# Performance work log

Hardware: AMD Instinct MI355X
Metric: run time of the kernel (lower is better)

## Reference

```python
import jax, jax.numpy as jnp
import numpy as np

N_G, E_G = 50000, 800000
N_S, E_S = 10000, 160000
NF = 64
B = 8

def _w(key, shape):
    fan_in = shape[-1]
    return jax.random.normal(key, shape, dtype=jnp.float32) / np.sqrt(fan_in)

def setup_inputs() -> dict:
    key = jax.random.key(0)
    ks = jax.random.split(key, 40)
    inp = {
        "graph_x": jax.random.normal(ks[0], (N_G, NF), dtype=jnp.float32),
        "subgraph_x": jax.random.normal(ks[1], (N_S, NF), dtype=jnp.float32),
        "point": jax.random.normal(ks[2], (B, NF), dtype=jnp.float32),
        "graph_edge_index": jax.random.randint(ks[3], (2, E_G), 0, N_G),
        "graph_batch": jnp.sort(jax.random.randint(ks[4], (N_G,), 0, B)),
        "subgraph_edge_index": jax.random.randint(ks[5], (2, E_S), 0, N_S),
        "subgraph_batch": jnp.sort(jax.random.randint(ks[6], (N_S,), 0, B)),
    }
    # GraphConv params per branch: channel sizes 64->128->256->192
    dims = [(2 * NF, NF), (4 * NF, 2 * NF), (3 * NF, 4 * NF)]
    i = 7
    for pre in ("g", "s"):
        for li, (o, c) in enumerate(dims, start=1):
            inp[f"{pre}W{li}r"] = _w(ks[i], (o, c)); i += 1  # lin_rel (aggregated)
            inp[f"{pre}W{li}n"] = _w(ks[i], (o, c)); i += 1  # lin_root (self)
            inp[f"{pre}B{li}"] = jnp.zeros((o,), dtype=jnp.float32)
    inp["l1W"] = _w(ks[i], (600, 3 * NF + 3 * NF + NF)); i += 1
    inp["l1b"] = jnp.zeros((600,), dtype=jnp.float32)
    inp["l2W"] = _w(ks[i], (256, 600)); i += 1
    inp["l2b"] = jnp.zeros((256,), dtype=jnp.float32)
    inp["l3W"] = _w(ks[i], (NF, 256)); i += 1
    inp["l3b"] = jnp.zeros((NF,), dtype=jnp.float32)
    return inp

def _graph_conv(x, src, dst, Wr, Wn, b, n_nodes):
    # PyG GraphConv: out_i = Wr @ sum_{j->i} x_j + Wn @ x_i + b
    agg = jax.ops.segment_sum(x[src], dst, num_segments=n_nodes)
    return agg @ Wr.T + x @ Wn.T + b

def _scatter_mean(x, seg, num_segments):
    s = jax.ops.segment_sum(x, seg, num_segments=num_segments)
    cnt = jax.ops.segment_sum(jnp.ones((x.shape[0],), x.dtype), seg, num_segments=num_segments)
    return s / jnp.maximum(cnt, 1.0)[:, None]

def _branch(x, edge_index, batch, params, n_nodes):
    src, dst = edge_index[0], edge_index[1]
    for (Wr, Wn, b) in params:
        x = jax.nn.elu(_graph_conv(x, src, dst, Wr, Wn, b, n_nodes))
    return _scatter_mean(x, batch, B)

def reference(graph_x, subgraph_x, point,
              gW1r, gW1n, gB1, gW2r, gW2n, gB2, gW3r, gW3n, gB3,
              sW1r, sW1n, sB1, sW2r, sW2n, sB2, sW3r, sW3n, sB3,
              l1W, l1b, l2W, l2b, l3W, l3b,
              graph_edge_index, graph_batch, subgraph_edge_index, subgraph_batch):
    x1 = _branch(graph_x, graph_edge_index, graph_batch,
                 [(gW1r, gW1n, gB1), (gW2r, gW2n, gB2), (gW3r, gW3n, gB3)], N_G)
    x2 = _branch(subgraph_x, subgraph_edge_index, subgraph_batch,
                 [(sW1r, sW1n, sB1), (sW2r, sW2n, sB2), (sW3r, sW3n, sB3)], N_S)
    x = jnp.concatenate([x1, x2, point], axis=-1)  # [B, 448]
    x = jax.nn.relu(x @ l1W.T + l1b)
    x = jax.nn.relu(x @ l2W.T + l2b)
    return x @ l3W.T + l3b  # [B, 64]
```

## Files before the change

kernel.cpp:

```cpp
#include <hip/hip_runtime.h>
#include <cmath>

typedef __attribute__((ext_vector_type(8))) short short8;
typedef __attribute__((ext_vector_type(4))) short shortx4;
typedef __attribute__((ext_vector_type(4))) float floatx4;
typedef __attribute__((ext_vector_type(2))) float floatx2;
typedef __attribute__((ext_vector_type(4))) int intx4;

#define N_G 50000
#define E_G 800000
#define N_S 10000
#define E_S 160000
#define NT (N_G + N_S)
#define ET (E_G + E_S)
#define BATCH 8
#define STRIDE 64
#define FPASS 8

__device__ __forceinline__ float b2f(short s) {
    unsigned u = ((unsigned)(unsigned short)s) << 16;
    return __builtin_bit_cast(float, u);
}
__device__ __forceinline__ short f2b(float f) {
    unsigned u = __builtin_bit_cast(unsigned, f);
    u += 0x7FFF + ((u >> 16) & 1);
    return (short)(u >> 16);
}

struct RepArgs { const float* Wr[6]; const float* Wn[6]; short* dst[6]; int cin[6]; int nk[6]; int groups[6]; };
__global__ void init_kernel(const float* __restrict__ gx, const float* __restrict__ sx,
                            short* __restrict__ X0, unsigned char* __restrict__ X0_8,
                            int* __restrict__ dcount, float* __restrict__ pooled,
                            const int* __restrict__ g_batch, const int* __restrict__ s_batch,
                            int* __restrict__ starts, RepArgs ra, int total_groups) {
    int t = blockIdx.x * blockDim.x + threadIdx.x;
    if (t < NT * 16) {
        size_t e = (size_t)t * 4;
        const float* src = (e < (size_t)N_G * 64) ? (gx + e) : (sx + (e - (size_t)N_G * 64));
        floatx4 v = *(const floatx4*)src;
        shortx4 o;
        o[0] = f2b(v[0]); o[1] = f2b(v[1]); o[2] = f2b(v[2]); o[3] = f2b(v[3]);
        *(shortx4*)(X0 + e) = o;
        int w8 = 0;
        w8 = __builtin_amdgcn_cvt_pk_fp8_f32(v[0], v[1], w8, false);
        w8 = __builtin_amdgcn_cvt_pk_fp8_f32(v[2], v[3], w8, true);
        *(unsigned int*)(X0_8 + e) = (unsigned int)w8;
    }
    if (t < NT) dcount[t] = 0;
    if (t < 16 * 192) pooled[t] = 0.f;
    if (t <= 16) {
        int b = t;
        if (b == 16) { starts[16] = NT; }
        else {
            int key, n, base;
            const int* arr;
            if (b < 8) { arr = g_batch; n = N_G; key = b; base = 0; }
            else       { arr = s_batch; n = N_S; key = b - 8; base = N_G; }
            int lo = 0, hi = n;
            while (lo < hi) { int mid = (lo + hi) >> 1; if (arr[mid] < key) lo = mid + 1; else hi = mid; }
            starts[b] = base + lo;
        }
    }
    if (t < total_groups) {
        int seg = 0, off = t;
        while (seg < 5 && off >= ra.groups[seg]) { off -= ra.groups[seg]; ++seg; }
        int CIN = ra.cin[seg], NK = ra.nk[seg];
        int lane = off & 63;
        int rest = off >> 6;
        int tt = rest % NK;
        int ot = rest / NK;
        int o = ot * 16 + (lane & 15);
        int kk = tt * 32 + (lane >> 4) * 8;
        const float* src = (kk < CIN) ? (ra.Wr[seg] + (size_t)o * CIN + kk)
                                      : (ra.Wn[seg] + (size_t)o * CIN + (kk - CIN));
        floatx4 u0 = *(const floatx4*)src;
        floatx4 u1 = *(const floatx4*)(src + 4);
        short8 d;
        d[0]=f2b(u0[0]); d[1]=f2b(u0[1]); d[2]=f2b(u0[2]); d[3]=f2b(u0[3]);
        d[4]=f2b(u1[0]); d[5]=f2b(u1[1]); d[6]=f2b(u1[2]); d[7]=f2b(u1[3]);
        *(short8*)(ra.dst[seg] + (size_t)off * 8) = d;
    }
}

__global__ void fill_kernel(const int* __restrict__ g_ei, const int* __restrict__ s_ei,
                            int* __restrict__ dcount, int* __restrict__ csr) {
    int pass = blockIdx.x & (FPASS - 1);
    int lb   = blockIdx.x >> 3;
    int t = lb * blockDim.x + threadIdx.x;
    if (t >= ET) return;
    int dst;
    if (t < E_G) dst = g_ei[E_G + t];
    else         dst = s_ei[E_S + (t - E_G)] + N_G;
    int lo = pass * (NT / FPASS);
    int hi = lo + (NT / FPASS);
    if (dst < lo || dst >= hi) return;
    int src;
    if (t < E_G) src = g_ei[t];
    else         src = s_ei[t - E_G] + N_G;
    int slot = atomicAdd(&dcount[dst], 1);
    if (slot < STRIDE) csr[(size_t)dst * STRIDE + slot] = src;
}

template<int C>
__global__ void agg8_kernel(const unsigned char* __restrict__ x8, const int* __restrict__ dcount,
                            const int* __restrict__ csr, short* __restrict__ out) {
    constexpr int C16 = C / 16;
    int t = blockIdx.x * blockDim.x + threadIdx.x;
    if (t >= NT * C16) return;
    int node = t / C16;
    int ch   = t % C16;
    int e0 = node * STRIDE;
    int e1 = e0 + min(dcount[node], STRIDE);
    float acc[16];
    #pragma unroll
    for (int j = 0; j < 16; ++j) acc[j] = 0.f;
    for (int e = e0; e < e1; ++e) {
        int s = csr[e];
        intx4 w = *(const intx4*)(x8 + (size_t)s * C + ch * 16);
        #pragma unroll
        for (int q = 0; q < 4; ++q) {
            floatx2 f0 = __builtin_amdgcn_cvt_pk_f32_fp8(w[q], false);
            floatx2 f1 = __builtin_amdgcn_cvt_pk_f32_fp8(w[q], true);
            acc[q * 4 + 0] += f0[0];
            acc[q * 4 + 1] += f0[1];
            acc[q * 4 + 2] += f1[0];
            acc[q * 4 + 3] += f1[1];
        }
    }
    short8 o0, o1;
    #pragma unroll
    for (int j = 0; j < 8; ++j) { o0[j] = f2b(acc[j]); o1[j] = f2b(acc[8 + j]); }
    short8* q = (short8*)(out + (size_t)node * C + ch * 16);
    q[0] = o0; q[1] = o1;
}

template<int CIN, int COUT, bool POOL>
__global__ __launch_bounds__(256) void gemm_elu_kernel(
        const short* __restrict__ A1, const short* __restrict__ A2,
        const short* __restrict__ gWF, const short* __restrict__ sWF,
        const float* __restrict__ gB, const float* __restrict__ sB,
        short* __restrict__ out, unsigned char* __restrict__ out8,
        float* __restrict__ pooled, const int* __restrict__ starts) {
    constexpr int NK  = CIN / 16;
    constexpr int NOT = COUT / 16;
    int wave = (blockIdx.x * blockDim.x + threadIdx.x) >> 6;
    int lane = threadIdx.x & 63;
    int r0 = wave * 16;
    if (r0 >= NT) return;
    bool sub = (r0 >= N_G);
    const short* WF = sub ? sWF : gWF;
    const float* bias = sub ? sB : gB;
    int id = lane & 15, quad = lane >> 4;
    int arow = r0 + id;
    short8 a[NK];
    #pragma unroll
    for (int t = 0; t < NK; ++t) {
        int kk = t * 32 + quad * 8;
        const short* p = (kk < CIN) ? (A1 + (size_t)arow * CIN + kk)
                                    : (A2 + (size_t)arow * CIN + (kk - CIN));
        a[t] = *(const short8*)p;
    }
    int seg0 = 0, seg1 = 0;
    bool uniform = true;
    if (POOL) {
        while (seg0 < 15 && starts[seg0 + 1] <= r0) ++seg0;
        seg1 = seg0;
        while (seg1 < 15 && starts[seg1 + 1] <= r0 + 15) ++seg1;
        uniform = (seg0 == seg1);
    }
    for (int ot = 0; ot < NOT; ++ot) {
        floatx4 acc = {0.f, 0.f, 0.f, 0.f};
        const short* wp = WF + (((size_t)ot * NK) * 64 + lane) * 8;
        #pragma unroll
        for (int t = 0; t < NK; ++t) {
            short8 b = *(const short8*)(wp + (size_t)t * 64 * 8);
            acc = __builtin_amdgcn_mfma_f32_16x16x32_bf16(a[t], b, acc, 0, 0, 0);
        }
        int o = ot * 16 + id;
        float bv = bias[o];
        float vr[4];
        #pragma unroll
        for (int r = 0; r < 4; ++r) {
            float v = acc[r] + bv;
            vr[r] = (v > 0.f) ? v : (expf(v) - 1.f);
        }
        if (!POOL) {
            #pragma unroll
            for (int r = 0; r < 4; ++r) {
                int nrow = r0 + quad * 4 + r;
                out[(size_t)nrow * COUT + o] = f2b(vr[r]);
                if (out8) {
                    int w8 = __builtin_amdgcn_cvt_pk_fp8_f32(vr[r], vr[r], 0, false);
                    out8[(size_t)nrow * COUT + o] = (unsigned char)(w8 & 0xFF);
                }
            }
        } else if (uniform) {
            float vsum = vr[0] + vr[1] + vr[2] + vr[3];
            vsum += __shfl_down(vsum, 32, 64);
            vsum += __shfl_down(vsum, 16, 64);
            if (lane < 16) atomicAdd(&pooled[seg0 * 192 + o], vsum);
        } else {
            #pragma unroll
            for (int r = 0; r < 4; ++r) {
                int nrow = r0 + quad * 4 + r;
                int sg = seg0;
                while (sg < seg1 && starts[sg + 1] <= nrow) ++sg;
                atomicAdd(&pooled[sg * 192 + o], vr[r]);
            }
        }
    }
}

__global__ void build_in_kernel(const float* __restrict__ pooled, const int* __restrict__ starts,
                                const float* __restrict__ point, float* __restrict__ mlp_in) {
    int t = blockIdx.x * blockDim.x + threadIdx.x;
    if (t >= BATCH * 448) return;
    int b = t / 448, j = t % 448;
    float v;
    if (j < 192) {
        int c = starts[b + 1] - starts[b];
        v = pooled[b * 192 + j] / (float)max(c, 1);
    } else if (j < 384) {
        int c = starts[9 + b] - starts[8 + b];
        v = pooled[(8 + b) * 192 + (j - 192)] / (float)max(c, 1);
    } else {
        v = point[b * 64 + (j - 384)];
    }
    mlp_in[t] = v;
}

__global__ __launch_bounds__(256) void dense_wave_kernel(
        const float* __restrict__ in, const float* __restrict__ W,
        const float* __restrict__ bias, float* __restrict__ out,
        int I, int O, int relu) {
    int wave = (blockIdx.x * blockDim.x + threadIdx.x) >> 6;
    int lane = threadIdx.x & 63;
    if (wave >= BATCH * O) return;
    int b = wave / O, o = wave % O;
    const float* x = in + (size_t)b * I;
    const float* w = W + (size_t)o * I;
    float acc = 0.f;
    for (int i = lane; i < I; i += 64) acc += x[i] * w[i];
    #pragma unroll
    for (int off = 32; off > 0; off >>= 1) acc += __shfl_down(acc, off, 64);
    if (lane == 0) {
        acc += bias[o];
        if (relu) acc = fmaxf(acc, 0.f);
        out[wave] = acc;
    }
}

extern "C" void kernel_launch(void* const* d_in, const int* in_sizes, int n_in,
                              void* d_out, int out_size, void* d_ws, size_t ws_size,
                              hipStream_t stream) {
    const float* graph_x = (const float*)d_in[0];
    const float* sub_x   = (const float*)d_in[1];
    const float* point   = (const float*)d_in[2];
    const int*   g_ei    = (const int*)d_in[3];
    const int*   g_batch = (const int*)d_in[4];
    const int*   s_ei    = (const int*)d_in[5];
    const int*   s_batch = (const int*)d_in[6];
    const float* gB1=(const float*)d_in[9],  *gB2=(const float*)d_in[12], *gB3=(const float*)d_in[15];
    const float* sB1=(const float*)d_in[18], *sB2=(const float*)d_in[21], *sB3=(const float*)d_in[24];
    const float* l1W=(const float*)d_in[25], *l1b=(const float*)d_in[26];
    const float* l2W=(const float*)d_in[27], *l2b=(const float*)d_in[28];
    const float* l3W=(const float*)d_in[29], *l3b=(const float*)d_in[30];

    char* ws = (char*)d_ws;
    size_t off = 0;
    auto alloc = [&](size_t bytes) -> char* {
        char* p = ws + off;
        off = (off + bytes + 255) & ~(size_t)255;
        return p;
    };
    int* dcount = (int*)alloc((size_t)NT * 4);
    int* csr = (int*)alloc((size_t)NT * STRIDE * 4);

    const int fsz[3] = {128 * 2 * 64, 256 * 2 * 128, 192 * 2 * 256};
    short* wfrag = (short*)alloc((size_t)(fsz[0] + fsz[1] + fsz[2]) * 2 * 2);
    short* gWF[3], *sWF[3];
    { size_t o2 = 0;
      for (int l = 0; l < 3; ++l) { gWF[l] = wfrag + o2; o2 += fsz[l]; }
      for (int l = 0; l < 3; ++l) { sWF[l] = wfrag + o2; o2 += fsz[l]; } }

    short* X0  = (short*)alloc((size_t)NT * 64 * 2);
    unsigned char* X0_8 = (unsigned char*)alloc((size_t)NT * 64);
    short* agg = (short*)alloc((size_t)NT * 256 * 2);
    short* h1  = (short*)alloc((size_t)NT * 128 * 2);
    short* h2  = (short*)alloc((size_t)NT * 256 * 2);
    unsigned char* h1_8 = (unsigned char*)alloc((size_t)NT * 128);
    unsigned char* h2_8 = (unsigned char*)alloc((size_t)NT * 256);

    float* pooled = (float*)alloc(16 * 192 * 4);
    int* starts = (int*)alloc(17 * 4);
    float* mlp_in = (float*)alloc(BATCH * 448 * 4);
    float* mlp_h1 = (float*)alloc(BATCH * 600 * 4);
    float* mlp_h2 = (float*)alloc(BATCH * 256 * 4);

    RepArgs ra;
    const int cin_l[3] = {64, 128, 256};
    const int nk_l[3]  = {4, 8, 16};
    const int not_l[3] = {8, 16, 12};
    const int wr_idx[6] = {7, 10, 13, 16, 19, 22};
    int total_groups = 0;
    for (int s = 0; s < 6; ++s) {
        int l = s % 3;
        ra.Wr[s] = (const float*)d_in[wr_idx[s]];
        ra.Wn[s] = (const float*)d_in[wr_idx[s] + 1];
        ra.dst[s] = (s < 3) ? gWF[l] : sWF[l];
        ra.cin[s] = cin_l[l];
        ra.nk[s] = nk_l[l];
        ra.groups[s] = not_l[l] * nk_l[l] * 64;
        total_groups += ra.groups[s];
    }

    init_kernel<<<(NT * 16 + 255) / 256, 256, 0, stream>>>(graph_x, sub_x, X0, X0_8, dcount,
                                                           pooled, g_batch, s_batch, starts,
                                                           ra, total_groups);

    fill_kernel<<<((ET + 255) / 256) * FPASS, 256, 0, stream>>>(g_ei, s_ei, dcount, csr);

    constexpr int NW = NT / 16;
    const int gemm_blocks = (NW + 3) / 4;

    agg8_kernel<64><<<(NT * 4 + 255) / 256, 256, 0, stream>>>(X0_8, dcount, csr, agg);
    gemm_elu_kernel<64, 128, false><<<gemm_blocks, 256, 0, stream>>>(agg, X0, gWF[0], sWF[0], gB1, sB1, h1, h1_8, nullptr, nullptr);
    agg8_kernel<128><<<(NT * 8 + 255) / 256, 256, 0, stream>>>(h1_8, dcount, csr, agg);
    gemm_elu_kernel<128, 256, false><<<gemm_blocks, 256, 0, stream>>>(agg, h1, gWF[1], sWF[1], gB2, sB2, h2, h2_8, nullptr, nullptr);
    agg8_kernel<256><<<(NT * 16 + 255) / 256, 256, 0, stream>>>(h2_8, dcount, csr, agg);
    gemm_elu_kernel<256, 192, true><<<gemm_blocks, 256, 0, stream>>>(agg, h2, gWF[2], sWF[2], gB3, sB3, nullptr, nullptr, pooled, starts);

    build_in_kernel<<<(BATCH * 448 + 255) / 256, 256, 0, stream>>>(pooled, starts, point, mlp_in);
    dense_wave_kernel<<<(BATCH * 600 + 3) / 4, 256, 0, stream>>>(mlp_in, l1W, l1b, mlp_h1, 448, 600, 1);
    dense_wave_kernel<<<(BATCH * 256 + 3) / 4, 256, 0, stream>>>(mlp_h1, l2W, l2b, mlp_h2, 600, 256, 1);
    dense_wave_kernel<<<(BATCH * 64 + 3) / 4, 256, 0, stream>>>(mlp_h2, l3W, l3b, (float*)d_out, 256, 64, 0);
}
```

Baseline: 391.4 us.

## Stage GraphConv weight tiles in LDS and split output channels across grid

Replaces the per-wave GEMM, which streamed every weight fragment from global memory for each 16-row tile, with a kernel that copies a slice of output-channel weights into shared memory once per block. Each wave now handles two row tiles. The grid is split over output-channel groups (y) and over the graph/subgraph branch (z). This is meant to cut repeated global weight traffic and raise reuse of each loaded weight fragment. In exchange, the A rows are reloaded once per channel group, and the launch bound of one block per SM plus larger register arrays may lower occupancy.

```diff
diff --git a/kernel.cpp b/kernel.cpp
--- a/kernel.cpp
+++ b/kernel.cpp
@@ -134,78 +134,99 @@
     q[0] = o0; q[1] = o1;
 }
 
-template<int CIN, int COUT, bool POOL>
-__global__ __launch_bounds__(256) void gemm_elu_kernel(
+template<int CIN, int COUT, int OTN, int RPW, bool POOL>
+__global__ __launch_bounds__(256, 1) void gemm_lds_kernel(
         const short* __restrict__ A1, const short* __restrict__ A2,
         const short* __restrict__ gWF, const short* __restrict__ sWF,
         const float* __restrict__ gB, const float* __restrict__ sB,
         short* __restrict__ out, unsigned char* __restrict__ out8,
         float* __restrict__ pooled, const int* __restrict__ starts) {
-    constexpr int NK  = CIN / 16;
-    constexpr int NOT = COUT / 16;
-    int wave = (blockIdx.x * blockDim.x + threadIdx.x) >> 6;
-    int lane = threadIdx.x & 63;
-    int r0 = wave * 16;
-    if (r0 >= NT) return;
-    bool sub = (r0 >= N_G);
-    const short* WF = sub ? sWF : gWF;
-    const float* bias = sub ? sB : gB;
+    constexpr int NK = CIN / 16;
+    __shared__ short lds[OTN * NK * 512];
+    int z = blockIdx.z;
+    const short* WF = z ? sWF : gWF;
+    const float* bias = z ? sB : gB;
+    int rowBase  = z ? N_G : 0;
+    int rowTiles = z ? (N_S / 16) : (N_G / 16);
+    int rtBase = blockIdx.x * (4 * RPW);
+    if (rtBase >= rowTiles) return;
+    const short* wsrc = WF + ((size_t)(blockIdx.y * OTN) * NK) * 512;
+    for (int i = threadIdx.x; i < OTN * NK * 64; i += 256)
+        *(short8*)(lds + (size_t)i * 8) = *(const short8*)(wsrc + (size_t)i * 8);
+    __syncthreads();
+    int wv = threadIdx.x >> 6, lane = threadIdx.x & 63;
     int id = lane & 15, quad = lane >> 4;
-    int arow = r0 + id;
-    short8 a[NK];
+    int rt[RPW]; bool act[RPW];
+    short8 a[RPW][NK];
     #pragma unroll
-    for (int t = 0; t < NK; ++t) {
-        int kk = t * 32 + quad * 8;
-        const short* p = (kk < CIN) ? (A1 + (size_t)arow * CIN + kk)
-                                    : (A2 + (size_t)arow * CIN + (kk - CIN));
-        a[t] = *(const short8*)p;
-    }
-    int seg0 = 0, seg1 = 0;
-    bool uniform = true;
+    for (int r = 0; r < RPW; ++r) {
+        rt[r] = rtBase + wv * RPW + r;
+        act[r] = rt[r] < rowTiles;
+        int arow = rowBase + (act[r] ? rt[r] : 0) * 16 + id;
+        #pragma unroll
+        for (int t = 0; t < NK; ++t) {
+            int kk = t * 32 + quad * 8;
+            const short* p = (kk < CIN) ? (A1 + (size_t)arow * CIN + kk)
+                                        : (A2 + (size_t)arow * CIN + (kk - CIN));
+            a[r][t] = *(const short8*)p;
+        }
+    }
+    int seg0[RPW], seg1[RPW];
     if (POOL) {
-        while (seg0 < 15 && starts[seg0 + 1] <= r0) ++seg0;
-        seg1 = seg0;
-        while (seg1 < 15 && starts[seg1 + 1] <= r0 + 15) ++seg1;
-        uniform = (seg0 == seg1);
-    }
-    for (int ot = 0; ot < NOT; ++ot) {
-        floatx4 acc = {0.f, 0.f, 0.f, 0.f};
-        const short* wp = WF + (((size_t)ot * NK) * 64 + lane) * 8;
-        #pragma unroll
-        for (int t = 0; t < NK; ++t) {
-            short8 b = *(const short8*)(wp + (size_t)t * 64 * 8);
-            acc = __builtin_amdgcn_mfma_f32_16x16x32_bf16(a[t], b, acc, 0, 0, 0);
-        }
-        int o = ot * 16 + id;
+        #pragma unroll
+        for (int r = 0; r < RPW; ++r) {
+            int r0 = rowBase + (act[r] ? rt[r] : 0) * 16;
+            int s0 = 0;
+            while (s0 < 15 && starts[s0 + 1] <= r0) ++s0;
+            int s1 = s0;
+            while (s1 < 15 && starts[s1 + 1] <= r0 + 15) ++s1;
+            seg0[r] = s0; seg1[r] = s1;
+        }
+    }
+    for (int oi = 0; oi < OTN; ++oi) {
+        short8 b[NK];
+        #pragma unroll
+        for (int t = 0; t < NK; ++t)
+            b[t] = *(const short8*)(lds + (((size_t)(oi * NK + t)) * 64 + lane) * 8);
+        int o = (blockIdx.y * OTN + oi) * 16 + id;
         float bv = bias[o];
-        float vr[4];
-        #pragma unroll
-        for (int r = 0; r < 4; ++r) {
-            float v = acc[r] + bv;
-            vr[r] = (v > 0.f) ? v : (expf(v) - 1.f);
-        }
-        if (!POOL) {
+        #pragma unroll
+        for (int r = 0; r < RPW; ++r) {
+            if (!act[r]) continue;
+            floatx4 acc = {0.f, 0.f, 0.f, 0.f};
             #pragma unroll
-            for (int r = 0; r < 4; ++r) {
-                int nrow = r0 + quad * 4 + r;
-                out[(size_t)nrow * COUT + o] = f2b(vr[r]);
-                if (out8) {
-                    int w8 = __builtin_amdgcn_cvt_pk_fp8_f32(vr[r], vr[r], 0, false);
-                    out8[(size_t)nrow * COUT + o] = (unsigned char)(w8 & 0xFF);
+            for (int t = 0; t < NK; ++t)
+                acc = __builtin_amdgcn_mfma_f32_16x16x32_bf16(a[r][t], b[t], acc, 0, 0, 0);
+            float vr[4];
+            #pragma unroll
+            for (int q = 0; q < 4; ++q) {
+                float v = acc[q] + bv;
+                vr[q] = (v > 0.f) ? v : (expf(v) - 1.f);
+            }
+            int r0 = rowBase + rt[r] * 16;
+            if (!POOL) {
+                #pragma unroll
+                for (int q = 0; q < 4; ++q) {
+                    int nrow = r0 + quad * 4 + q;
+                    out[(size_t)nrow * COUT + o] = f2b(vr[q]);
+                    if (out8) {
+                        int w8 = __builtin_amdgcn_cvt_pk_fp8_f32(vr[q], vr[q], 0, false);
+                        out8[(size_t)nrow * COUT + o] = (unsigned char)(w8 & 0xFF);
+                    }
                 }
-            }
-        } else if (uniform) {
-            float vsum = vr[0] + vr[1] + vr[2] + vr[3];
-            vsum += __shfl_down(vsum, 32, 64);
-            vsum += __shfl_down(vsum, 16, 64);
-            if (lane < 16) atomicAdd(&pooled[seg0 * 192 + o], vsum);
-        } else {
-            #pragma unroll
-            for (int r = 0; r < 4; ++r) {
-                int nrow = r0 + quad * 4 + r;
-                int sg = seg0;
-                while (sg < seg1 && starts[sg + 1] <= nrow) ++sg;
-                atomicAdd(&pooled[sg * 192 + o], vr[r]);
+            } else if (seg0[r] == seg1[r]) {
+                float vsum = vr[0] + vr[1] + vr[2] + vr[3];
+                vsum += __shfl_down(vsum, 32, 64);
+                vsum += __shfl_down(vsum, 16, 64);
+                if (lane < 16) atomicAdd(&pooled[seg0[r] * 192 + o], vsum);
+            } else {
+                #pragma unroll
+                for (int q = 0; q < 4; ++q) {
+                    int nrow = r0 + quad * 4 + q;
+                    int sg = seg0[r];
+                    while (sg < seg1[r] && starts[sg + 1] <= nrow) ++sg;
+                    atomicAdd(&pooled[sg * 192 + o], vr[q]);
+                }
             }
         }
     }
@@ -320,15 +341,17 @@
 
     fill_kernel<<<((ET + 255) / 256) * FPASS, 256, 0, stream>>>(g_ei, s_ei, dcount, csr);
 
-    constexpr int NW = NT / 16;
-    const int gemm_blocks = (NW + 3) / 4;
+    const int gx = (3125 + 7) / 8;
 
     agg8_kernel<64><<<(NT * 4 + 255) / 256, 256, 0, stream>>>(X0_8, dcount, csr, agg);
-    gemm_elu_kernel<64, 128, false><<<gemm_blocks, 256, 0, stream>>>(agg, X0, gWF[0], sWF[0], gB1, sB1, h1, h1_8, nullptr, nullptr);
+    gemm_lds_kernel<64, 128, 8, 2, false><<<dim3(gx, 1, 2), 256, 0, stream>>>(
+        agg, X0, gWF[0], sWF[0], gB1, sB1, h1, h1_8, nullptr, nullptr);
     agg8_kernel<128><<<(NT * 8 + 255) / 256, 256, 0, stream>>>(h1_8, dcount, csr, agg);
-    gemm_elu_kernel<128, 256, false><<<gemm_blocks, 256, 0, stream>>>(agg, h1, gWF[1], sWF[1], gB2, sB2, h2, h2_8, nullptr, nullptr);
+    gemm_lds_kernel<128, 256, 8, 2, false><<<dim3(gx, 2, 2), 256, 0, stream>>>(
+        agg, h1, gWF[1], sWF[1], gB2, sB2, h2, h2_8, nullptr, nullptr);
     agg8_kernel<256><<<(NT * 16 + 255) / 256, 256, 0, stream>>>(h2_8, dcount, csr, agg);
-    gemm_elu_kernel<256, 192, true><<<gemm_blocks, 256, 0, stream>>>(agg, h2, gWF[2], sWF[2], gB3, sB3, nullptr, nullptr, pooled, starts);
+    gemm_lds_kernel<256, 192, 4, 2, true><<<dim3(gx, 3, 2), 256, 0, stream>>>(
+        agg, h2, gWF[2], sWF[2], gB3, sB3, nullptr, nullptr, pooled, starts);
 
     build_in_kernel<<<(BATCH * 448 + 255) / 256, 256, 0, stream>>>(pooled, starts, point, mlp_in);
     dense_wave_kernel<<<(BATCH * 600 + 3) / 4, 256, 0, stream>>>(mlp_in, l1W, l1b, mlp_h1, 448, 600, 1);
```

New measurement: 410.4 us. 4.9% more time.

## Fuse neighbor aggregation into GEMM+ELU kernel via shared-memory staging

Applied to the files above, without the earlier changes.

Merges each layer's separate fp8 gather-aggregation kernel and bf16 MFMA GEMM kernel into one kernel. Per 64-row block, threads aggregate neighbor features into LDS, optionally stage the self features in LDS too, sync, then run the MFMA/ELU epilogue from LDS. This removes the global agg buffer round trip and three kernel launches. In exchange, each block's aggregation and GEMM phases are serialized, and the larger LDS footprint may lower occupancy.

```diff
diff --git a/kernel.cpp b/kernel.cpp
--- a/kernel.cpp
+++ b/kernel.cpp
@@ -101,72 +101,84 @@
     if (slot < STRIDE) csr[(size_t)dst * STRIDE + slot] = src;
 }
 
-template<int C>
-__global__ void agg8_kernel(const unsigned char* __restrict__ x8, const int* __restrict__ dcount,
-                            const int* __restrict__ csr, short* __restrict__ out) {
-    constexpr int C16 = C / 16;
-    int t = blockIdx.x * blockDim.x + threadIdx.x;
-    if (t >= NT * C16) return;
-    int node = t / C16;
-    int ch   = t % C16;
-    int e0 = node * STRIDE;
-    int e1 = e0 + min(dcount[node], STRIDE);
-    float acc[16];
-    #pragma unroll
-    for (int j = 0; j < 16; ++j) acc[j] = 0.f;
-    for (int e = e0; e < e1; ++e) {
-        int s = csr[e];
-        intx4 w = *(const intx4*)(x8 + (size_t)s * C + ch * 16);
-        #pragma unroll
-        for (int q = 0; q < 4; ++q) {
-            floatx2 f0 = __builtin_amdgcn_cvt_pk_f32_fp8(w[q], false);
-            floatx2 f1 = __builtin_amdgcn_cvt_pk_f32_fp8(w[q], true);
-            acc[q * 4 + 0] += f0[0];
-            acc[q * 4 + 1] += f0[1];
-            acc[q * 4 + 2] += f1[0];
-            acc[q * 4 + 3] += f1[1];
-        }
-    }
-    short8 o0, o1;
-    #pragma unroll
-    for (int j = 0; j < 8; ++j) { o0[j] = f2b(acc[j]); o1[j] = f2b(acc[8 + j]); }
-    short8* q = (short8*)(out + (size_t)node * C + ch * 16);
-    q[0] = o0; q[1] = o1;
-}
-
 template<int CIN, int COUT, bool POOL>
-__global__ __launch_bounds__(256) void gemm_elu_kernel(
-        const short* __restrict__ A1, const short* __restrict__ A2,
+__global__ __launch_bounds__(256) void fused_layer_kernel(
+        const unsigned char* __restrict__ x8, const short* __restrict__ hprev,
+        const int* __restrict__ dcount, const int* __restrict__ csr,
         const short* __restrict__ gWF, const short* __restrict__ sWF,
         const float* __restrict__ gB, const float* __restrict__ sB,
         short* __restrict__ out, unsigned char* __restrict__ out8,
         float* __restrict__ pooled, const int* __restrict__ starts) {
-    constexpr int NK  = CIN / 16;
-    constexpr int NOT = COUT / 16;
-    int wave = (blockIdx.x * blockDim.x + threadIdx.x) >> 6;
-    int lane = threadIdx.x & 63;
-    int r0 = wave * 16;
+    constexpr int NK   = CIN / 16;
+    constexpr int NOT  = COUT / 16;
+    constexpr bool STA2 = (CIN <= 128);
+    constexpr int WP   = STA2 ? (2 * CIN + 8) : (CIN + 8);
+    __shared__ short lds[64 * WP];
+    int rowBase = blockIdx.x * 64;
+    int tid = threadIdx.x;
+    constexpr int CH = CIN / 16;
+    for (int item = tid; item < 64 * CH; item += 256) {
+        int row = item / CH, ch = item % CH;
+        int grow = rowBase + row;
+        if (grow >= NT) continue;
+        int e0 = grow * STRIDE;
+        int e1 = e0 + min(dcount[grow], STRIDE);
+        float acc[16];
+        #pragma unroll
+        for (int j = 0; j < 16; ++j) acc[j] = 0.f;
+        for (int e = e0; e < e1; ++e) {
+            int s = csr[e];
+            intx4 w = *(const intx4*)(x8 + (size_t)s * CIN + ch * 16);
+            #pragma unroll
+            for (int q = 0; q < 4; ++q) {
+                floatx2 f0 = __builtin_amdgcn_cvt_pk_f32_fp8(w[q], false);
+                floatx2 f1 = __builtin_amdgcn_cvt_pk_f32_fp8(w[q], true);
+                acc[q * 4 + 0] += f0[0];
+                acc[q * 4 + 1] += f0[1];
+                acc[q * 4 + 2] += f1[0];
+                acc[q * 4 + 3] += f1[1];
+            }
+        }
+        short8 o0, o1;
+        #pragma unroll
+        for (int j = 0; j < 8; ++j) { o0[j] = f2b(acc[j]); o1[j] = f2b(acc[8 + j]); }
+        short* p = lds + row * WP + ch * 16;
+        *(short8*)p = o0;
+        *(short8*)(p + 8) = o1;
+    }
+    if (STA2) {
+        constexpr int CH2 = CIN / 8;
+        for (int item = tid; item < 64 * CH2; item += 256) {
+            int row = item / CH2, ch = item % CH2;
+            int grow = rowBase + row;
+            if (grow >= NT) continue;
+            *(short8*)(lds + row * WP + CIN + ch * 8) =
+                *(const short8*)(hprev + (size_t)grow * CIN + ch * 8);
+        }
+    }
+    __syncthreads();
+    int wv = tid >> 6, lane = tid & 63;
+    int r0 = rowBase + wv * 16;
     if (r0 >= NT) return;
     bool sub = (r0 >= N_G);
     const short* WF = sub ? sWF : gWF;
     const float* bias = sub ? sB : gB;
     int id = lane & 15, quad = lane >> 4;
-    int arow = r0 + id;
+    int lrow = wv * 16 + id;
     short8 a[NK];
     #pragma unroll
     for (int t = 0; t < NK; ++t) {
         int kk = t * 32 + quad * 8;
-        const short* p = (kk < CIN) ? (A1 + (size_t)arow * CIN + kk)
-                                    : (A2 + (size_t)arow * CIN + (kk - CIN));
-        a[t] = *(const short8*)p;
+        if (STA2 || kk < CIN)
+            a[t] = *(const short8*)(lds + lrow * WP + kk);
+        else
+            a[t] = *(const short8*)(hprev + (size_t)(r0 + id) * CIN + (kk - CIN));
     }
     int seg0 = 0, seg1 = 0;
-    bool uniform = true;
     if (POOL) {
         while (seg0 < 15 && starts[seg0 + 1] <= r0) ++seg0;
         seg1 = seg0;
         while (seg1 < 15 && starts[seg1 + 1] <= r0 + 15) ++seg1;
-        uniform = (seg0 == seg1);
     }
     for (int ot = 0; ot < NOT; ++ot) {
         floatx4 acc = {0.f, 0.f, 0.f, 0.f};
@@ -189,12 +201,10 @@
             for (int r = 0; r < 4; ++r) {
                 int nrow = r0 + quad * 4 + r;
                 out[(size_t)nrow * COUT + o] = f2b(vr[r]);
-                if (out8) {
-                    int w8 = __builtin_amdgcn_cvt_pk_fp8_f32(vr[r], vr[r], 0, false);
-                    out8[(size_t)nrow * COUT + o] = (unsigned char)(w8 & 0xFF);
-                }
+                int w8 = __builtin_amdgcn_cvt_pk_fp8_f32(vr[r], vr[r], 0, false);
+                out8[(size_t)nrow * COUT + o] = (unsigned char)(w8 & 0xFF);
             }
-        } else if (uniform) {
+        } else if (seg0 == seg1) {
             float vsum = vr[0] + vr[1] + vr[2] + vr[3];
             vsum += __shfl_down(vsum, 32, 64);
             vsum += __shfl_down(vsum, 16, 64);
@@ -285,7 +295,6 @@
 
     short* X0  = (short*)alloc((size_t)NT * 64 * 2);
     unsigned char* X0_8 = (unsigned char*)alloc((size_t)NT * 64);
-    short* agg = (short*)alloc((size_t)NT * 256 * 2);
     short* h1  = (short*)alloc((size_t)NT * 128 * 2);
     short* h2  = (short*)alloc((size_t)NT * 256 * 2);
     unsigned char* h1_8 = (unsigned char*)alloc((size_t)NT * 128);
@@ -320,15 +329,14 @@
 
     fill_kernel<<<((ET + 255) / 256) * FPASS, 256, 0, stream>>>(g_ei, s_ei, dcount, csr);
 
-    constexpr int NW = NT / 16;
-    const int gemm_blocks = (NW + 3) / 4;
-
-    agg8_kernel<64><<<(NT * 4 + 255) / 256, 256, 0, stream>>>(X0_8, dcount, csr, agg);
-    gemm_elu_kernel<64, 128, false><<<gemm_blocks, 256, 0, stream>>>(agg, X0, gWF[0], sWF[0], gB1, sB1, h1, h1_8, nullptr, nullptr);
-    agg8_kernel<128><<<(NT * 8 + 255) / 256, 256, 0, stream>>>(h1_8, dcount, csr, agg);
-    gemm_elu_kernel<128, 256, false><<<gemm_blocks, 256, 0, stream>>>(agg, h1, gWF[1], sWF[1], gB2, sB2, h2, h2_8, nullptr, nullptr);
-    agg8_kernel<256><<<(NT * 16 + 255) / 256, 256, 0, stream>>>(h2_8, dcount, csr, agg);
-    gemm_elu_kernel<256, 192, true><<<gemm_blocks, 256, 0, stream>>>(agg, h2, gWF[2], sWF[2], gB3, sB3, nullptr, nullptr, pooled, starts);
+    const int gx = (NT + 63) / 64;
+
+    fused_layer_kernel<64, 128, false><<<gx, 256, 0, stream>>>(
+        X0_8, X0, dcount, csr, gWF[0], sWF[0], gB1, sB1, h1, h1_8, nullptr, nullptr);
+    fused_layer_kernel<128, 256, false><<<gx, 256, 0, stream>>>(
+        h1_8, h1, dcount, csr, gWF[1], sWF[1], gB2, sB2, h2, h2_8, nullptr, nullptr);
+    fused_layer_kernel<256, 192, true><<<gx, 256, 0, stream>>>(
+        h2_8, h2, dcount, csr, gWF[2], sWF[2], gB3, sB3, nullptr, nullptr, pooled, starts);
 
     build_in_kernel<<<(BATCH * 448 + 255) / 256, 256, 0, stream>>>(pooled, starts, point, mlp_in);
     dense_wave_kernel<<<(BATCH * 600 + 3) / 4, 256, 0, stream>>>(mlp_in, l1W, l1b, mlp_h1, 448, 600, 1);
```

After: 395.3 us. About the same (+1.0%).

## Drop bf16 activation copies, read root features from fp8, fuse MLP input build

Applied to the files above, without the earlier changes.

The GEMM kernels now read the self/root operand from the fp8 activation buffers and convert it to bf16 in registers. The separate bf16 copies of X0, h1 and h2 are no longer written or read, which cuts global memory traffic. The build_in kernel is folded into the first MLP layer, saving one launch. The trade-off is lower precision on the root term, which was bf16 before and is now fp8, plus extra conversion instructions in the GEMM.

```diff
diff --git a/kernel.cpp b/kernel.cpp
--- a/kernel.cpp
+++ b/kernel.cpp
@@ -6,6 +6,7 @@
 typedef __attribute__((ext_vector_type(4))) float floatx4;
 typedef __attribute__((ext_vector_type(2))) float floatx2;
 typedef __attribute__((ext_vector_type(4))) int intx4;
+typedef __attribute__((ext_vector_type(2))) int intx2;
 
 #define N_G 50000
 #define E_G 800000
@@ -26,10 +27,20 @@
     u += 0x7FFF + ((u >> 16) & 1);
     return (short)(u >> 16);
 }
+__device__ __forceinline__ short8 fp8x8_to_bf16(intx2 w) {
+    floatx2 f0 = __builtin_amdgcn_cvt_pk_f32_fp8(w[0], false);
+    floatx2 f1 = __builtin_amdgcn_cvt_pk_f32_fp8(w[0], true);
+    floatx2 f2 = __builtin_amdgcn_cvt_pk_f32_fp8(w[1], false);
+    floatx2 f3 = __builtin_amdgcn_cvt_pk_f32_fp8(w[1], true);
+    short8 r;
+    r[0]=f2b(f0[0]); r[1]=f2b(f0[1]); r[2]=f2b(f1[0]); r[3]=f2b(f1[1]);
+    r[4]=f2b(f2[0]); r[5]=f2b(f2[1]); r[6]=f2b(f3[0]); r[7]=f2b(f3[1]);
+    return r;
+}
 
 struct RepArgs { const float* Wr[6]; const float* Wn[6]; short* dst[6]; int cin[6]; int nk[6]; int groups[6]; };
 __global__ void init_kernel(const float* __restrict__ gx, const float* __restrict__ sx,
-                            short* __restrict__ X0, unsigned char* __restrict__ X0_8,
+                            unsigned char* __restrict__ X0_8,
                             int* __restrict__ dcount, float* __restrict__ pooled,
                             const int* __restrict__ g_batch, const int* __restrict__ s_batch,
                             int* __restrict__ starts, RepArgs ra, int total_groups) {
@@ -38,9 +49,6 @@
         size_t e = (size_t)t * 4;
         const float* src = (e < (size_t)N_G * 64) ? (gx + e) : (sx + (e - (size_t)N_G * 64));
         floatx4 v = *(const floatx4*)src;
-        shortx4 o;
-        o[0] = f2b(v[0]); o[1] = f2b(v[1]); o[2] = f2b(v[2]); o[3] = f2b(v[3]);
-        *(shortx4*)(X0 + e) = o;
         int w8 = 0;
         w8 = __builtin_amdgcn_cvt_pk_fp8_f32(v[0], v[1], w8, false);
         w8 = __builtin_amdgcn_cvt_pk_fp8_f32(v[2], v[3], w8, true);
@@ -136,10 +144,10 @@
 
 template<int CIN, int COUT, bool POOL>
 __global__ __launch_bounds__(256) void gemm_elu_kernel(
-        const short* __restrict__ A1, const short* __restrict__ A2,
+        const short* __restrict__ A1, const unsigned char* __restrict__ A2_8,
         const short* __restrict__ gWF, const short* __restrict__ sWF,
         const float* __restrict__ gB, const float* __restrict__ sB,
-        short* __restrict__ out, unsigned char* __restrict__ out8,
+        unsigned char* __restrict__ out8,
         float* __restrict__ pooled, const int* __restrict__ starts) {
     constexpr int NK  = CIN / 16;
     constexpr int NOT = COUT / 16;
@@ -156,17 +164,18 @@
     #pragma unroll
     for (int t = 0; t < NK; ++t) {
         int kk = t * 32 + quad * 8;
-        const short* p = (kk < CIN) ? (A1 + (size_t)arow * CIN + kk)
-                                    : (A2 + (size_t)arow * CIN + (kk - CIN));
-        a[t] = *(const short8*)p;
+        if (kk < CIN) {
+            a[t] = *(const short8*)(A1 + (size_t)arow * CIN + kk);
+        } else {
+            intx2 w = *(const intx2*)(A2_8 + (size_t)arow * CIN + (kk - CIN));
+            a[t] = fp8x8_to_bf16(w);
+        }
     }
     int seg0 = 0, seg1 = 0;
-    bool uniform = true;
     if (POOL) {
         while (seg0 < 15 && starts[seg0 + 1] <= r0) ++seg0;
         seg1 = seg0;
         while (seg1 < 15 && starts[seg1 + 1] <= r0 + 15) ++seg1;
-        uniform = (seg0 == seg1);
     }
     for (int ot = 0; ot < NOT; ++ot) {
         floatx4 acc = {0.f, 0.f, 0.f, 0.f};
@@ -188,13 +197,10 @@
             #pragma unroll
             for (int r = 0; r < 4; ++r) {
                 int nrow = r0 + quad * 4 + r;
-                out[(size_t)nrow * COUT + o] = f2b(vr[r]);
-                if (out8) {
-                    int w8 = __builtin_amdgcn_cvt_pk_fp8_f32(vr[r], vr[r], 0, false);
-                    out8[(size_t)nrow * COUT + o] = (unsigned char)(w8 & 0xFF);
-                }
+                int w8 = __builtin_amdgcn_cvt_pk_fp8_f32(vr[r], vr[r], 0, false);
+                out8[(size_t)nrow * COUT + o] = (unsigned char)(w8 & 0xFF);
             }
-        } else if (uniform) {
+        } else if (seg0 == seg1) {
             float vsum = vr[0] + vr[1] + vr[2] + vr[3];
             vsum += __shfl_down(vsum, 32, 64);
             vsum += __shfl_down(vsum, 16, 64);
@@ -211,22 +217,28 @@
     }
 }
 
-__global__ void build_in_kernel(const float* __restrict__ pooled, const int* __restrict__ starts,
-                                const float* __restrict__ point, float* __restrict__ mlp_in) {
-    int t = blockIdx.x * blockDim.x + threadIdx.x;
-    if (t >= BATCH * 448) return;
-    int b = t / 448, j = t % 448;
-    float v;
-    if (j < 192) {
-        int c = starts[b + 1] - starts[b];
-        v = pooled[b * 192 + j] / (float)max(c, 1);
-    } else if (j < 384) {
-        int c = starts[9 + b] - starts[8 + b];
-        v = pooled[(8 + b) * 192 + (j - 192)] / (float)max(c, 1);
-    } else {
-        v = point[b * 64 + (j - 384)];
-    }
-    mlp_in[t] = v;
+__global__ __launch_bounds__(256) void mlp1_kernel(
+        const float* __restrict__ pooled, const int* __restrict__ starts,
+        const float* __restrict__ point, const float* __restrict__ W,
+        const float* __restrict__ bias, float* __restrict__ out) {
+    int wave = (blockIdx.x * blockDim.x + threadIdx.x) >> 6;
+    int lane = threadIdx.x & 63;
+    if (wave >= BATCH * 600) return;
+    int b = wave / 600, o = wave % 600;
+    float invg = 1.f / (float)max(starts[b + 1] - starts[b], 1);
+    float invs = 1.f / (float)max(starts[9 + b] - starts[8 + b], 1);
+    const float* w = W + (size_t)o * 448;
+    float acc = 0.f;
+    for (int i = lane; i < 448; i += 64) {
+        float x;
+        if (i < 192)      x = pooled[b * 192 + i] * invg;
+        else if (i < 384) x = pooled[(8 + b) * 192 + (i - 192)] * invs;
+        else              x = point[b * 64 + (i - 384)];
+        acc += x * w[i];
+    }
+    #pragma unroll
+    for (int off = 32; off > 0; off >>= 1) acc += __shfl_down(acc, off, 64);
+    if (lane == 0) out[wave] = fmaxf(acc + bias[o], 0.f);
 }
 
 __global__ __launch_bounds__(256) void dense_wave_kernel(
@@ -283,17 +295,13 @@
       for (int l = 0; l < 3; ++l) { gWF[l] = wfrag + o2; o2 += fsz[l]; }
       for (int l = 0; l < 3; ++l) { sWF[l] = wfrag + o2; o2 += fsz[l]; } }
 
-    short* X0  = (short*)alloc((size_t)NT * 64 * 2);
     unsigned char* X0_8 = (unsigned char*)alloc((size_t)NT * 64);
     short* agg = (short*)alloc((size_t)NT * 256 * 2);
-    short* h1  = (short*)alloc((size_t)NT * 128 * 2);
-    short* h2  = (short*)alloc((size_t)NT * 256 * 2);
     unsigned char* h1_8 = (unsigned char*)alloc((size_t)NT * 128);
     unsigned char* h2_8 = (unsigned char*)alloc((size_t)NT * 256);
 
     float* pooled = (float*)alloc(16 * 192 * 4);
     int* starts = (int*)alloc(17 * 4);
-    float* mlp_in = (float*)alloc(BATCH * 448 * 4);
     float* mlp_h1 = (float*)alloc(BATCH * 600 * 4);
     float* mlp_h2 = (float*)alloc(BATCH * 256 * 4);
 
@@ -314,7 +322,7 @@
         total_groups += ra.groups[s];
     }
 
-    init_kernel<<<(NT * 16 + 255) / 256, 256, 0, stream>>>(graph_x, sub_x, X0, X0_8, dcount,
+    init_kernel<<<(NT * 16 + 255) / 256, 256, 0, stream>>>(graph_x, sub_x, X0_8, dcount,
                                                            pooled, g_batch, s_batch, starts,
                                                            ra, total_groups);
 
@@ -324,14 +332,16 @@
     const int gemm_blocks = (NW + 3) / 4;
 
     agg8_kernel<64><<<(NT * 4 + 255) / 256, 256, 0, stream>>>(X0_8, dcount, csr, agg);
-    gemm_elu_kernel<64, 128, false><<<gemm_blocks, 256, 0, stream>>>(agg, X0, gWF[0], sWF[0], gB1, sB1, h1, h1_8, nullptr, nullptr);
+    gemm_elu_kernel<64, 128, false><<<gemm_blocks, 256, 0, stream>>>(
+        agg, X0_8, gWF[0], sWF[0], gB1, sB1, h1_8, nullptr, nullptr);
     agg8_kernel<128><<<(NT * 8 + 255) / 256, 256, 0, stream>>>(h1_8, dcount, csr, agg);
-    gemm_elu_kernel<128, 256, false><<<gemm_blocks, 256, 0, stream>>>(agg, h1, gWF[1], sWF[1], gB2, sB2, h2, h2_8, nullptr, nullptr);
+    gemm_elu_kernel<128, 256, false><<<gemm_blocks, 256, 0, stream>>>(
+        agg, h1_8, gWF[1], sWF[1], gB2, sB2, h2_8, nullptr, nullptr);
     agg8_kernel<256><<<(NT * 16 + 255) / 256, 256, 0, stream>>>(h2_8, dcount, csr, agg);
-    gemm_elu_kernel<256, 192, true><<<gemm_blocks, 256, 0, stream>>>(agg, h2, gWF[2], sWF[2], gB3, sB3, nullptr, nullptr, pooled, starts);
-
-    build_in_kernel<<<(BATCH * 448 + 255) / 256, 256, 0, stream>>>(pooled, starts, point, mlp_in);
-    dense_wave_kernel<<<(BATCH * 600 + 3) / 4, 256, 0, stream>>>(mlp_in, l1W, l1b, mlp_h1, 448, 600, 1);
+    gemm_elu_kernel<256, 192, true><<<gemm_blocks, 256, 0, stream>>>(
+        agg, h2_8, gWF[2], sWF[2], gB3, sB3, nullptr, pooled, starts);
+
+    mlp1_kernel<<<(BATCH * 600 + 3) / 4, 256, 0, stream>>>(pooled, starts, point, l1W, l1b, mlp_h1);
     dense_wave_kernel<<<(BATCH * 256 + 3) / 4, 256, 0, stream>>>(mlp_h1, l2W, l2b, mlp_h2, 600, 256, 1);
     dense_wave_kernel<<<(BATCH * 64 + 3) / 4, 256, 0, stream>>>(mlp_h2, l3W, l3b, (float*)d_out, 256, 64, 0);
 }
```

After: 383.1 us. 2.1% less time.
